# Kernel optimization log

Hardware: AMD Instinct MI355X
Metric: run time of the kernel (lower is better)

Reference implementation:

```python
import jax, jax.numpy as jnp
import numpy as np
from jax import lax

B, T = 256, 64
X_DIMS, CCG_DIMS, H, N_TAG = 512, 256, 1024, 512
DIN = X_DIMS + CCG_DIMS
PAD = 0


def setup_inputs() -> dict:
    key = jax.random.key(0)
    ks = jax.random.split(key, 12)
    emb = jax.random.normal(ks[0], (N_TAG, CCG_DIMS), jnp.float32)
    emb = emb.at[PAD].set(0.0)  # padding_idx row is zero
    s_ih = 1.0 / np.sqrt(H)
    return {
        "x": jax.random.normal(ks[1], (B, X_DIMS), jnp.float32),
        "atom_truth": jax.random.randint(ks[2], (B, T), 0, N_TAG),
        "atom_mask": jax.random.randint(ks[3], (B, T), 0, 2).astype(bool),
        "emb": emb,
        "W_ih": jax.random.normal(ks[4], (4 * H, DIN), jnp.float32) * s_ih,
        "W_hh": jax.random.normal(ks[5], (4 * H, H), jnp.float32) * s_ih,
        "b_ih": jax.random.normal(ks[6], (4 * H,), jnp.float32) * s_ih,
        "b_hh": jax.random.normal(ks[7], (4 * H,), jnp.float32) * s_ih,
        "W_out": jax.random.normal(ks[8], (N_TAG, H), jnp.float32) * s_ih,
        "b_out": jax.random.normal(ks[9], (N_TAG,), jnp.float32) * s_ih,
        "h0": jax.random.normal(ks[10], (B, H), jnp.float32),
        "c0": jax.random.normal(ks[11], (B, H), jnp.float32),
    }


def reference(x, atom_truth, atom_mask, emb, W_ih, W_hh, b_ih, b_hh, W_out, b_out, h0, c0):
    b, t = atom_truth.shape
    # teacher forcing: step 0 uses token 0, step k uses atom_truth[:, k-1]
    prev_tok = jnp.concatenate([jnp.zeros((b, 1), atom_truth.dtype), atom_truth[:, :-1]], axis=1)
    ccg = emb[prev_tok]                                      # [B,T,E]
    inp = jnp.concatenate([jnp.broadcast_to(x[:, None, :], (b, t, x.shape[1])), ccg], axis=-1)
    # precompute input projection for all steps: [B,T,4H]
    xproj = jnp.einsum('btd,gd->btg', inp, W_ih) + b_ih + b_hh

    def cell(carry, xt):                                     # xt: [B,4H]
        h, c = carry
        gates = xt + h @ W_hh.T
        i, f, g, o = jnp.split(gates, 4, axis=-1)            # torch gate order i,f,g,o
        i, f, o = jax.nn.sigmoid(i), jax.nn.sigmoid(f), jax.nn.sigmoid(o)
        g = jnp.tanh(g)
        c = f * c + i * g
        h = o * jnp.tanh(c)
        return (h, c), h

    _, hs = lax.scan(cell, (h0, c0), jnp.swapaxes(xproj, 0, 1))  # hs: [T,B,H]
    logits = hs @ W_out.T + b_out                            # [T,B,N_TAG]
    logp = jax.nn.log_softmax(logits, axis=-1)
    tgt = atom_truth.T                                       # [T,B]
    nll = -jnp.take_along_axis(logp, tgt[..., None], axis=-1)[..., 0]  # [T,B]
    mask = atom_mask.T.astype(nll.dtype)
    return jnp.sum(nll * mask) / jnp.sum(mask)


if __name__ == "__main__":
    print(reference(**setup_inputs()))
```

## Files before the change

### kernel.cpp

```cpp
#include <hip/hip_runtime.h>
#include <hip/hip_bf16.h>

#define BB 256
#define TT 64
#define XD 512
#define CCG 256
#define DINk 768
#define HH 1024
#define G4 4096
#define NTAG 512

typedef float f32x4 __attribute__((ext_vector_type(4)));
typedef short s16x8 __attribute__((ext_vector_type(8)));
typedef short s16x4 __attribute__((ext_vector_type(4)));

#define WS_HS    0ull
#define WS_XBASE (WS_HS + (size_t)(TT+1)*BB*HH*2)
#define WS_EPROJ (WS_XBASE + (size_t)BB*G4*4)
#define WS_WIH   (WS_EPROJ + (size_t)NTAG*G4*4)
#define WS_WOUT  (WS_WIH + (size_t)G4*DINk*2)
#define WS_XBF   (WS_WOUT + (size_t)NTAG*HH*2)
#define WS_EMBBF (WS_XBF + (size_t)BB*XD*2)
#define WS_CNT   (WS_EMBBF + (size_t)NTAG*CCG*2)
#define WS_ACC   (WS_CNT + 1024)
#define WS_FLAG  (WS_ACC + 64)
#define WS_XPROJ (WS_FLAG + 64)

static __device__ __forceinline__ short f2bf(float f) {
  __hip_bfloat16 h = __float2bfloat16(f);
  return __builtin_bit_cast(short, h);
}
static __device__ __forceinline__ float bf2f(unsigned short u) {
  unsigned x = ((unsigned)u) << 16;
  return __builtin_bit_cast(float, x);
}
static __device__ __forceinline__ void store_dword_cc(void* p, unsigned v) {
  asm volatile("global_store_dword %0, %1, off sc0 sc1" :: "v"(p), "v"(v) : "memory");
}
static __device__ __forceinline__ void store_short_cc(void* p, unsigned v) {
  asm volatile("global_store_short %0, %1, off sc0 sc1" :: "v"(p), "v"(v) : "memory");
}
static __device__ __forceinline__ int load_int_cc(const void* p) {
  int r;
  asm volatile("global_load_dword %0, %1, off sc0 sc1\n\ts_waitcnt vmcnt(0)"
               : "=v"(r) : "v"(p) : "memory");
  return r;
}
static __device__ __forceinline__ float fsig(float x) {
  return __builtin_amdgcn_rcpf(1.f + __expf(-x));
}
static __device__ __forceinline__ float ftanh(float x) {
  return 1.f - 2.f * __builtin_amdgcn_rcpf(1.f + __expf(2.f * x));
}

__global__ void k_f2bf8(const float* __restrict__ in, short* __restrict__ out, int n8) {
  int i = blockIdx.x * blockDim.x + threadIdx.x;
  if (i >= n8) return;
  size_t idx = (size_t)i * 8;
  float4 a = *(const float4*)(in + idx);
  float4 b = *(const float4*)(in + idx + 4);
  s16x8 o;
  o[0]=f2bf(a.x); o[1]=f2bf(a.y); o[2]=f2bf(a.z); o[3]=f2bf(a.w);
  o[4]=f2bf(b.x); o[5]=f2bf(b.y); o[6]=f2bf(b.z); o[7]=f2bf(b.w);
  *(s16x8*)(out + idx) = o;
}

__global__ void k_init(const float* __restrict__ h0, const int* __restrict__ mask_as_int,
                       char* __restrict__ ws) {
  int tid = blockIdx.x * blockDim.x + threadIdx.x;
  short* hb0 = (short*)(ws + WS_HS);
  for (int i = tid; i < BB * HH; i += gridDim.x * blockDim.x) hb0[i] = f2bf(h0[i]);
  if (blockIdx.x == 0) {
    int* cnt = (int*)(ws + WS_CNT);
    for (int i = threadIdx.x; i < 256; i += blockDim.x) cnt[i] = 0;
    int v = 0;
    for (int i = threadIdx.x; i < 4096; i += blockDim.x) v |= (mask_as_int[i] & ~1);
    __shared__ int red[256];
    red[threadIdx.x] = v;
    __syncthreads();
    if (threadIdx.x == 0) {
      int a = 0;
      for (int j = 0; j < 256; j++) a |= red[j];
      ((int*)(ws + WS_FLAG))[0] = (a != 0) ? 1 : 0;
      float* acc = (float*)(ws + WS_ACC);
      acc[0] = 0.f; acc[1] = 0.f;
    }
  }
}

__global__ __launch_bounds__(256) void k_gemm(const short* __restrict__ A, int lda,
    const short* __restrict__ Bm, int ldb, int bcol0,
    short* __restrict__ C, int ldc, int ksteps,
    const float* __restrict__ bias1, const float* __restrict__ bias2) {
  int w = threadIdx.x >> 6, l = threadIdx.x & 63;
  int lc = l & 15, lq = l >> 4;
  int arow = blockIdx.x * 64 + w * 16 + lc;
  f32x4 acc[4];
  const f32x4 z = {0.f, 0.f, 0.f, 0.f};
#pragma unroll
  for (int i = 0; i < 4; i++) acc[i] = z;
  const short* ap = A + (size_t)arow * lda + lq * 8;
  for (int kk = 0; kk < ksteps; ++kk) {
    s16x8 a = *(const s16x8*)(ap + kk * 32);
#pragma unroll
    for (int nt = 0; nt < 4; ++nt) {
      int brow = blockIdx.y * 64 + nt * 16 + lc;
      s16x8 b = *(const s16x8*)(Bm + (size_t)brow * ldb + bcol0 + kk * 32 + lq * 8);
      acc[nt] = __builtin_amdgcn_mfma_f32_16x16x32_bf16(a, b, acc[nt], 0, 0, 0);
    }
  }
#pragma unroll
  for (int nt = 0; nt < 4; ++nt) {
    int col = blockIdx.y * 64 + nt * 16 + lc;
    float badd = (bias1 ? bias1[col] : 0.f) + (bias2 ? bias2[col] : 0.f);
#pragma unroll
    for (int j = 0; j < 4; j++) {
      int r = blockIdx.x * 64 + w * 16 + lq * 4 + j;
      C[(size_t)r * ldc + col] = f2bf(acc[nt][j] + badd);
    }
  }
}

__global__ __launch_bounds__(256) void k_xproj_t(const short* __restrict__ xb,
    const short* __restrict__ ep, const int* __restrict__ atruth,
    short* __restrict__ out) {
  __shared__ short tile[64 * 264];
  const int cc = blockIdx.x, g = blockIdx.y, t = blockIdx.z;
  const int b = threadIdx.x;
  const int tok = (t == 0) ? 0 : atruth[b * TT + t - 1];
  const int gc0 = g * 1024 + cc * 64;
  const short* xs = xb + (size_t)b * G4 + gc0;
  const short* es = ep + (size_t)tok * G4 + gc0;
#pragma unroll
  for (int i = 0; i < 64; i += 8) {
    s16x8 xv = *(const s16x8*)(xs + i);
    s16x8 ev = *(const s16x8*)(es + i);
#pragma unroll
    for (int j = 0; j < 8; ++j)
      tile[(i + j) * 264 + b] = f2bf(bf2f((unsigned short)xv[j]) + bf2f((unsigned short)ev[j]));
  }
  __syncthreads();
  const int c = threadIdx.x >> 2, b0 = (threadIdx.x & 3) * 64;
  short* dst = out + ((size_t)t * G4 + gc0 + c) * BB + b0;
  const short* src = tile + c * 264 + b0;
#pragma unroll
  for (int i = 0; i < 64; i += 8) *(s16x8*)(dst + i) = *(const s16x8*)(src + i);
}

__global__ __launch_bounds__(512, 2) void k_lstm(const float* __restrict__ Whh,
    const short* __restrict__ xproj, const float* __restrict__ c0,
    char* __restrict__ ws) {
  extern __shared__ char sm[];
  float* part = (float*)sm;
  const int bid = blockIdx.x;
  const int xcd = bid & 7, slot = bid >> 3;
  const int mg = xcd >> 1;
  const int hb = slot * 2 + (xcd & 1);
  const int wgid = (xcd & 1) * 32 + slot;
  const int tid = threadIdx.x;
  const int w = tid >> 6, l = tid & 63;
  const int lc = l & 15, lq = l >> 4;
  const int wy = w & 1, kq = w >> 1;

  const int colbase = hb * 16;
  short* hs = (short*)(ws + WS_HS);
  int* flags = (int*)(ws + WS_CNT);
  const int arow0 = mg * 64 + wy * 32;

  s16x8 breg[4][8];
#pragma unroll
  for (int g = 0; g < 4; ++g) {
    const float* wr = Whh + (size_t)(g * HH + colbase + lc) * HH + kq * 256 + lq * 8;
#pragma unroll
    for (int s = 0; s < 8; ++s) {
      float4 f0 = *(const float4*)(wr + s * 32);
      float4 f1 = *(const float4*)(wr + s * 32 + 4);
      s16x8 o;
      o[0]=f2bf(f0.x); o[1]=f2bf(f0.y); o[2]=f2bf(f0.z); o[3]=f2bf(f0.w);
      o[4]=f2bf(f1.x); o[5]=f2bf(f1.y); o[6]=f2bf(f1.z); o[7]=f2bf(f1.w);
      breg[g][s] = o;
    }
  }

  float cst[2][4];
  if (kq == 0) {
#pragma unroll
    for (int rt = 0; rt < 2; ++rt)
#pragma unroll
      for (int j = 0; j < 4; ++j)
        cst[rt][j] = c0[(size_t)(arow0 + rt * 16 + lq * 4 + j) * HH + colbase + lc];
  }

  for (int t = 0; t < TT; ++t) {
    s16x4 xg[2][4];
    if (kq == 0) {
#pragma unroll
      for (int rt = 0; rt < 2; ++rt)
#pragma unroll
        for (int g = 0; g < 4; ++g)
          xg[rt][g] = *(const s16x4*)(xproj +
              ((size_t)t * G4 + g * HH + colbase + lc) * BB + arow0 + rt * 16 + lq * 4);
    }

    if (t && w == 0) {
      const int* f = flags + mg * 64 + l;
      for (;;) {
        int v = load_int_cc(f);
        if (__all(v >= t)) break;
        __builtin_amdgcn_s_sleep(1);
      }
    }
    __syncthreads();

    const f32x4 z = {0.f, 0.f, 0.f, 0.f};
    f32x4 acc[2][4];
#pragma unroll
    for (int rt = 0; rt < 2; ++rt)
#pragma unroll
      for (int g = 0; g < 4; ++g) acc[rt][g] = z;
    const short* ab = hs + (size_t)t * (BB * HH) + (size_t)(arow0 + lc) * HH + kq * 256 + lq * 8;
#pragma unroll
    for (int s = 0; s < 8; ++s) {
      s16x8 a0 = *(const s16x8*)(ab + s * 32);
      s16x8 a1 = *(const s16x8*)(ab + 16 * HH + s * 32);
#pragma unroll
      for (int g = 0; g < 4; ++g) {
        acc[0][g] = __builtin_amdgcn_mfma_f32_16x16x32_bf16(a0, breg[g][s], acc[0][g], 0, 0, 0);
        acc[1][g] = __builtin_amdgcn_mfma_f32_16x16x32_bf16(a1, breg[g][s], acc[1][g], 0, 0, 0);
      }
    }

    if (kq) {
      float* ps = part + (size_t)(((kq - 1) * 2 + wy) * 64 + l) * 36;
#pragma unroll
      for (int rt = 0; rt < 2; ++rt)
#pragma unroll
        for (int g = 0; g < 4; ++g)
          *(f32x4*)(ps + (rt * 4 + g) * 4) = acc[rt][g];
    }
    __syncthreads();

    if (kq == 0) {
#pragma unroll
      for (int q = 0; q < 3; ++q) {
        const float* ps = part + (size_t)((q * 2 + wy) * 64 + l) * 36;
#pragma unroll
        for (int rt = 0; rt < 2; ++rt)
#pragma unroll
          for (int g = 0; g < 4; ++g)
            acc[rt][g] += *(const f32x4*)(ps + (rt * 4 + g) * 4);
      }
#pragma unroll
      for (int rt = 0; rt < 2; ++rt) {
        short* hrow = hs + (size_t)(t + 1) * (BB * HH) +
                      (size_t)(arow0 + rt * 16 + lq * 4) * HH + colbase + lc;
#pragma unroll
        for (int j = 0; j < 4; ++j) {
          float pi = acc[rt][0][j] + bf2f((unsigned short)xg[rt][0][j]);
          float pf = acc[rt][1][j] + bf2f((unsigned short)xg[rt][1][j]);
          float pg = acc[rt][2][j] + bf2f((unsigned short)xg[rt][2][j]);
          float po = acc[rt][3][j] + bf2f((unsigned short)xg[rt][3][j]);
          float cv = fsig(pf) * cst[rt][j] + fsig(pi) * ftanh(pg);
          cst[rt][j] = cv;
          store_short_cc(hrow + (size_t)j * HH, (unsigned)(unsigned short)f2bf(fsig(po) * ftanh(cv)));
        }
      }
    }
    asm volatile("s_waitcnt vmcnt(0)" ::: "memory");
    __syncthreads();
    if (tid == 0 && t < TT - 1) store_dword_cc(flags + mg * 64 + wgid, t + 1);
  }
}

__global__ __launch_bounds__(256, 1) void k_logits(const short* __restrict__ hsb,
    const short* __restrict__ Wo, const float* __restrict__ bout,
    const int* __restrict__ atruth, const void* __restrict__ maskp,
    char* __restrict__ ws) {
  extern __shared__ char sm[];
  const int tid = threadIdx.x;
  const int w = tid >> 6, l = tid & 63;
  const int lc = l & 15, lq = l >> 4;
  const int rowbase = blockIdx.x * 64 + w * 16;
  f32x4 acc[32];
#pragma unroll
  for (int nt = 0; nt < 32; ++nt) {
    float bv = bout[nt * 16 + lc];
    f32x4 tmp = {bv, bv, bv, bv};
    acc[nt] = tmp;
  }
  const int swzl = (lc & 7) << 4;
  for (int kb = 0; kb < 16; ++kb) {
    __syncthreads();
    {
      const int r0 = tid >> 3, q = tid & 7;
#pragma unroll
      for (int i = 0; i < 16; i++) {
        int r = r0 + 32 * i;
        s16x8 v = *(const s16x8*)(Wo + (size_t)r * HH + kb * 64 + q * 8);
        *(s16x8*)(sm + r * 128 + ((q * 16) ^ ((r & 7) << 4))) = v;
      }
    }
    __syncthreads();
#pragma unroll
    for (int ks = 0; ks < 2; ++ks) {
      s16x8 a = *(const s16x8*)(hsb + (size_t)(rowbase + lc) * HH + kb * 64 + ks * 32 + lq * 8);
      const int kx = (ks * 64 + lq * 16) ^ swzl;
#pragma unroll
      for (int nt = 0; nt < 32; ++nt) {
        s16x8 b = *(const s16x8*)(sm + (nt * 16 + lc) * 128 + kx);
        acc[nt] = __builtin_amdgcn_mfma_f32_16x16x32_bf16(a, b, acc[nt], 0, 0, 0);
      }
    }
  }
  const int bytemode = ((const int*)(ws + WS_FLAG))[0];
  const unsigned char* mb = (const unsigned char*)maskp;
  const int* mi = (const int*)maskp;
  float nlls = 0.f, cnts = 0.f;
#pragma unroll
  for (int j = 0; j < 4; j++) {
    int gr = rowbase + lq * 4 + j;
    int tt = gr >> 8, b = gr & 255;
    float m = -1e30f;
#pragma unroll
    for (int nt = 0; nt < 32; ++nt) m = fmaxf(m, acc[nt][j]);
    m = fmaxf(m, __shfl_xor(m, 1)); m = fmaxf(m, __shfl_xor(m, 2));
    m = fmaxf(m, __shfl_xor(m, 4)); m = fmaxf(m, __shfl_xor(m, 8));
    float s = 0.f;
#pragma unroll
    for (int nt = 0; nt < 32; ++nt) s += __expf(acc[nt][j] - m);
    s += __shfl_xor(s, 1); s += __shfl_xor(s, 2);
    s += __shfl_xor(s, 4); s += __shfl_xor(s, 8);
    float lse = m + __logf(s);
    int tg = atruth[b * TT + tt];
    int mk = bytemode ? (int)mb[b * TT + tt] : mi[b * TT + tt];
    if (((tg & 15) == lc) && mk) {
      float tl = 0.f;
#pragma unroll
      for (int nt = 0; nt < 32; ++nt) if (nt == (tg >> 4)) tl = acc[nt][j];
      nlls += (lse - tl);
    }
    if (lc == 0 && mk) cnts += 1.f;
  }
#pragma unroll
  for (int off = 1; off < 64; off <<= 1) {
    nlls += __shfl_xor(nlls, off);
    cnts += __shfl_xor(cnts, off);
  }
  if (l == 0) {
    float* accf = (float*)(ws + WS_ACC);
    atomicAdd(&accf[0], nlls);
    atomicAdd(&accf[1], cnts);
  }
}

__global__ void k_final(const char* __restrict__ ws, float* __restrict__ out) {
  const float* accf = (const float*)(ws + WS_ACC);
  out[0] = accf[0] / accf[1];
}

extern "C" void kernel_launch(void* const* d_in, const int* in_sizes, int n_in,
                              void* d_out, int out_size, void* d_ws, size_t ws_size,
                              hipStream_t stream) {
  const float* x      = (const float*)d_in[0];
  const int*   atruth = (const int*)d_in[1];
  const void*  amask  = d_in[2];
  const float* emb    = (const float*)d_in[3];
  const float* W_ih   = (const float*)d_in[4];
  const float* W_hh   = (const float*)d_in[5];
  const float* b_ih   = (const float*)d_in[6];
  const float* b_hh   = (const float*)d_in[7];
  const float* W_out  = (const float*)d_in[8];
  const float* b_out  = (const float*)d_in[9];
  const float* h0     = (const float*)d_in[10];
  const float* c0     = (const float*)d_in[11];
  char* ws = (char*)d_ws;
  float* out = (float*)d_out;

  hipFuncSetAttribute((const void*)k_lstm, hipFuncAttributeMaxDynamicSharedMemorySize, 55296);
  hipFuncSetAttribute((const void*)k_logits, hipFuncAttributeMaxDynamicSharedMemorySize, 65536);

  k_f2bf8<<<dim3((G4 * DINk / 8 + 255) / 256), 256, 0, stream>>>(W_ih, (short*)(ws + WS_WIH), G4 * DINk / 8);
  k_f2bf8<<<dim3((NTAG * HH / 8 + 255) / 256), 256, 0, stream>>>(W_out, (short*)(ws + WS_WOUT), NTAG * HH / 8);
  k_f2bf8<<<dim3((BB * XD / 8 + 255) / 256), 256, 0, stream>>>(x, (short*)(ws + WS_XBF), BB * XD / 8);
  k_f2bf8<<<dim3((NTAG * CCG / 8 + 255) / 256), 256, 0, stream>>>(emb, (short*)(ws + WS_EMBBF), NTAG * CCG / 8);

  k_init<<<64, 256, 0, stream>>>(h0, (const int*)amask, ws);

  k_gemm<<<dim3(4, 64), 256, 0, stream>>>((short*)(ws + WS_XBF), XD, (short*)(ws + WS_WIH), DINk, 0,
                                          (short*)(ws + WS_XBASE), G4, XD / 32, b_ih, b_hh);
  k_gemm<<<dim3(8, 64), 256, 0, stream>>>((short*)(ws + WS_EMBBF), CCG, (short*)(ws + WS_WIH), DINk, XD,
                                          (short*)(ws + WS_EPROJ), G4, CCG / 32, nullptr, nullptr);

  k_xproj_t<<<dim3(16, 4, 64), 256, 0, stream>>>((const short*)(ws + WS_XBASE),
                                                 (const short*)(ws + WS_EPROJ), atruth,
                                                 (short*)(ws + WS_XPROJ));

  k_lstm<<<256, 512, 55296, stream>>>(W_hh, (const short*)(ws + WS_XPROJ), c0, ws);

  k_logits<<<256, 256, 65536, stream>>>((short*)(ws + WS_HS) + BB * HH, (short*)(ws + WS_WOUT), b_out,
                                        atruth, amask, ws);
  k_final<<<1, 1, 0, stream>>>(ws, out);
}
```

Measured before the change: 628.7 us.

## Fuse token-gathered input projection into LSTM kernel and retile to 32x32 blocks

Drops the separate pre-transposed per-timestep projection kernel and its large intermediate buffer. The LSTM kernel now keeps the constant x-projection for its own rows in registers. Each step it prefetches the embedding-projection rows for the next token into shared memory. Blocks are retiled to 32 batch rows by 32 hidden columns, so the inter-block flag barrier covers groups of 32 blocks instead of 64, and the cross-wave reduction plus gate epilogue is split across two waves instead of one. The larger shared-memory footprint (about 80 KB) may limit residency to one block per CU, and adds a per-step dependent token load.

```diff
diff --git a/kernel.cpp b/kernel.cpp
--- a/kernel.cpp
+++ b/kernel.cpp
@@ -24,7 +24,6 @@
 #define WS_CNT   (WS_EMBBF + (size_t)NTAG*CCG*2)
 #define WS_ACC   (WS_CNT + 1024)
 #define WS_FLAG  (WS_ACC + 64)
-#define WS_XPROJ (WS_FLAG + 64)
 
 static __device__ __forceinline__ short f2bf(float f) {
   __hip_bfloat16 h = __float2bfloat16(f);
@@ -121,56 +120,32 @@
   }
 }
 
-__global__ __launch_bounds__(256) void k_xproj_t(const short* __restrict__ xb,
-    const short* __restrict__ ep, const int* __restrict__ atruth,
-    short* __restrict__ out) {
-  __shared__ short tile[64 * 264];
-  const int cc = blockIdx.x, g = blockIdx.y, t = blockIdx.z;
-  const int b = threadIdx.x;
-  const int tok = (t == 0) ? 0 : atruth[b * TT + t - 1];
-  const int gc0 = g * 1024 + cc * 64;
-  const short* xs = xb + (size_t)b * G4 + gc0;
-  const short* es = ep + (size_t)tok * G4 + gc0;
-#pragma unroll
-  for (int i = 0; i < 64; i += 8) {
-    s16x8 xv = *(const s16x8*)(xs + i);
-    s16x8 ev = *(const s16x8*)(es + i);
-#pragma unroll
-    for (int j = 0; j < 8; ++j)
-      tile[(i + j) * 264 + b] = f2bf(bf2f((unsigned short)xv[j]) + bf2f((unsigned short)ev[j]));
-  }
-  __syncthreads();
-  const int c = threadIdx.x >> 2, b0 = (threadIdx.x & 3) * 64;
-  short* dst = out + ((size_t)t * G4 + gc0 + c) * BB + b0;
-  const short* src = tile + c * 264 + b0;
-#pragma unroll
-  for (int i = 0; i < 64; i += 8) *(s16x8*)(dst + i) = *(const s16x8*)(src + i);
-}
-
 __global__ __launch_bounds__(512, 2) void k_lstm(const float* __restrict__ Whh,
-    const short* __restrict__ xproj, const float* __restrict__ c0,
+    const short* __restrict__ xbase, const short* __restrict__ eproj,
+    const int* __restrict__ atruth, const float* __restrict__ c0,
     char* __restrict__ ws) {
   extern __shared__ char sm[];
   float* part = (float*)sm;
+  short* xbuf = (short*)(sm + 73728);
   const int bid = blockIdx.x;
   const int xcd = bid & 7, slot = bid >> 3;
-  const int mg = xcd >> 1;
-  const int hb = slot * 2 + (xcd & 1);
-  const int wgid = (xcd & 1) * 32 + slot;
+  const int grp = (xcd >> 1) * 2 + (slot & 1);
+  const int id  = (xcd & 1) * 16 + (slot >> 1);
+  const int row0 = grp * 32;
+  const int colbase = id * 32;
   const int tid = threadIdx.x;
   const int w = tid >> 6, l = tid & 63;
   const int lc = l & 15, lq = l >> 4;
-  const int wy = w & 1, kq = w >> 1;
-
-  const int colbase = hb * 16;
+  const int ct = w & 1, kq = w >> 1;
+  const int col0 = colbase + ct * 16;
+
   short* hs = (short*)(ws + WS_HS);
   int* flags = (int*)(ws + WS_CNT);
-  const int arow0 = mg * 64 + wy * 32;
 
   s16x8 breg[4][8];
 #pragma unroll
   for (int g = 0; g < 4; ++g) {
-    const float* wr = Whh + (size_t)(g * HH + colbase + lc) * HH + kq * 256 + lq * 8;
+    const float* wr = Whh + (size_t)(g * HH + col0 + lc) * HH + kq * 256 + lq * 8;
 #pragma unroll
     for (int s = 0; s < 8; ++s) {
       float4 f0 = *(const float4*)(wr + s * 32);
@@ -182,28 +157,26 @@
     }
   }
 
-  float cst[2][4];
-  if (kq == 0) {
-#pragma unroll
-    for (int rt = 0; rt < 2; ++rt)
-#pragma unroll
-      for (int j = 0; j < 4; ++j)
-        cst[rt][j] = c0[(size_t)(arow0 + rt * 16 + lq * 4 + j) * HH + colbase + lc];
-  }
+  float cst[4], xbf[4][4];
+  if (kq < 2) {
+#pragma unroll
+    for (int j = 0; j < 4; ++j) {
+      int r = row0 + kq * 16 + lq * 4 + j;
+      cst[j] = c0[(size_t)r * HH + col0 + lc];
+#pragma unroll
+      for (int g = 0; g < 4; ++g)
+        xbf[g][j] = bf2f((unsigned short)xbase[(size_t)r * G4 + g * HH + col0 + lc]);
+    }
+  }
+
+  const int gr = tid >> 4;
+  const int p16 = tid & 15;
+  const size_t ep_off = (size_t)(p16 >> 2) * HH + colbase + (p16 & 3) * 8;
+  s16x8 ev = *(const s16x8*)(eproj + ep_off);
 
   for (int t = 0; t < TT; ++t) {
-    s16x4 xg[2][4];
-    if (kq == 0) {
-#pragma unroll
-      for (int rt = 0; rt < 2; ++rt)
-#pragma unroll
-        for (int g = 0; g < 4; ++g)
-          xg[rt][g] = *(const s16x4*)(xproj +
-              ((size_t)t * G4 + g * HH + colbase + lc) * BB + arow0 + rt * 16 + lq * 4);
-    }
-
     if (t && w == 0) {
-      const int* f = flags + mg * 64 + l;
+      const int* f = flags + grp * 32 + (l & 31);
       for (;;) {
         int v = load_int_cc(f);
         if (__all(v >= t)) break;
@@ -212,13 +185,19 @@
     }
     __syncthreads();
 
+    *(s16x8*)(xbuf + gr * 132 + p16 * 8) = ev;
+    if (t + 1 < TT) {
+      int tokv = atruth[(row0 + gr) * TT + t];
+      ev = *(const s16x8*)(eproj + (size_t)tokv * G4 + ep_off);
+    }
+
     const f32x4 z = {0.f, 0.f, 0.f, 0.f};
     f32x4 acc[2][4];
 #pragma unroll
     for (int rt = 0; rt < 2; ++rt)
 #pragma unroll
       for (int g = 0; g < 4; ++g) acc[rt][g] = z;
-    const short* ab = hs + (size_t)t * (BB * HH) + (size_t)(arow0 + lc) * HH + kq * 256 + lq * 8;
+    const short* ab = hs + (size_t)t * (BB * HH) + (size_t)(row0 + lc) * HH + kq * 256 + lq * 8;
 #pragma unroll
     for (int s = 0; s < 8; ++s) {
       s16x8 a0 = *(const s16x8*)(ab + s * 32);
@@ -230,45 +209,52 @@
       }
     }
 
-    if (kq) {
-      float* ps = part + (size_t)(((kq - 1) * 2 + wy) * 64 + l) * 36;
-#pragma unroll
-      for (int rt = 0; rt < 2; ++rt)
-#pragma unroll
-        for (int g = 0; g < 4; ++g)
-          *(f32x4*)(ps + (rt * 4 + g) * 4) = acc[rt][g];
-    }
-    __syncthreads();
-
-    if (kq == 0) {
-#pragma unroll
-      for (int q = 0; q < 3; ++q) {
-        const float* ps = part + (size_t)((q * 2 + wy) * 64 + l) * 36;
-#pragma unroll
-        for (int rt = 0; rt < 2; ++rt)
-#pragma unroll
-          for (int g = 0; g < 4; ++g)
-            acc[rt][g] += *(const f32x4*)(ps + (rt * 4 + g) * 4);
-      }
-#pragma unroll
-      for (int rt = 0; rt < 2; ++rt) {
-        short* hrow = hs + (size_t)(t + 1) * (BB * HH) +
-                      (size_t)(arow0 + rt * 16 + lq * 4) * HH + colbase + lc;
-#pragma unroll
-        for (int j = 0; j < 4; ++j) {
-          float pi = acc[rt][0][j] + bf2f((unsigned short)xg[rt][0][j]);
-          float pf = acc[rt][1][j] + bf2f((unsigned short)xg[rt][1][j]);
-          float pg = acc[rt][2][j] + bf2f((unsigned short)xg[rt][2][j]);
-          float po = acc[rt][3][j] + bf2f((unsigned short)xg[rt][3][j]);
-          float cv = fsig(pf) * cst[rt][j] + fsig(pi) * ftanh(pg);
-          cst[rt][j] = cv;
-          store_short_cc(hrow + (size_t)j * HH, (unsigned)(unsigned short)f2bf(fsig(po) * ftanh(cv)));
-        }
+    {
+      float* pb0 = part + (size_t)(((kq * 2 + ct) * 2 + 0) * 64 + l) * 18;
+      float* pb1 = part + (size_t)(((kq * 2 + ct) * 2 + 1) * 64 + l) * 18;
+      if (kq != 0) {
+#pragma unroll
+        for (int g = 0; g < 4; ++g) *(f32x4*)(pb0 + g * 4) = acc[0][g];
+      }
+      if (kq != 1) {
+#pragma unroll
+        for (int g = 0; g < 4; ++g) *(f32x4*)(pb1 + g * 4) = acc[1][g];
+      }
+    }
+    __syncthreads();
+
+    if (kq < 2) {
+      const int rt = kq;
+      f32x4 s0 = acc[rt][0], s1 = acc[rt][1], s2 = acc[rt][2], s3 = acc[rt][3];
+#pragma unroll
+      for (int q2 = 0; q2 < 4; ++q2) {
+        if (q2 == kq) continue;
+        const float* pb = part + (size_t)(((q2 * 2 + ct) * 2 + rt) * 64 + l) * 18;
+        s0 += *(const f32x4*)(pb);
+        s1 += *(const f32x4*)(pb + 4);
+        s2 += *(const f32x4*)(pb + 8);
+        s3 += *(const f32x4*)(pb + 12);
+      }
+      const unsigned short* xbu = (const unsigned short*)xbuf;
+      const int cc = ct * 16 + lc;
+      short* hbase = hs + (size_t)(t + 1) * (BB * HH);
+#pragma unroll
+      for (int j = 0; j < 4; ++j) {
+        int rr = kq * 16 + lq * 4 + j;
+        int xi = rr * 132;
+        float pi = s0[j] + bf2f(xbu[xi + cc])      + xbf[0][j];
+        float pf = s1[j] + bf2f(xbu[xi + 32 + cc]) + xbf[1][j];
+        float pg = s2[j] + bf2f(xbu[xi + 64 + cc]) + xbf[2][j];
+        float po = s3[j] + bf2f(xbu[xi + 96 + cc]) + xbf[3][j];
+        float cv = fsig(pf) * cst[j] + fsig(pi) * ftanh(pg);
+        cst[j] = cv;
+        store_short_cc(hbase + (size_t)(row0 + rr) * HH + col0 + lc,
+                       (unsigned)(unsigned short)f2bf(fsig(po) * ftanh(cv)));
       }
     }
     asm volatile("s_waitcnt vmcnt(0)" ::: "memory");
     __syncthreads();
-    if (tid == 0 && t < TT - 1) store_dword_cc(flags + mg * 64 + wgid, t + 1);
+    if (tid == 0 && t < TT - 1) store_dword_cc(flags + grp * 32 + id, t + 1);
   }
 }
 
@@ -376,7 +362,7 @@
   char* ws = (char*)d_ws;
   float* out = (float*)d_out;
 
-  hipFuncSetAttribute((const void*)k_lstm, hipFuncAttributeMaxDynamicSharedMemorySize, 55296);
+  hipFuncSetAttribute((const void*)k_lstm, hipFuncAttributeMaxDynamicSharedMemorySize, 82176);
   hipFuncSetAttribute((const void*)k_logits, hipFuncAttributeMaxDynamicSharedMemorySize, 65536);
 
   k_f2bf8<<<dim3((G4 * DINk / 8 + 255) / 256), 256, 0, stream>>>(W_ih, (short*)(ws + WS_WIH), G4 * DINk / 8);
@@ -391,11 +377,8 @@
   k_gemm<<<dim3(8, 64), 256, 0, stream>>>((short*)(ws + WS_EMBBF), CCG, (short*)(ws + WS_WIH), DINk, XD,
                                           (short*)(ws + WS_EPROJ), G4, CCG / 32, nullptr, nullptr);
 
-  k_xproj_t<<<dim3(16, 4, 64), 256, 0, stream>>>((const short*)(ws + WS_XBASE),
-                                                 (const short*)(ws + WS_EPROJ), atruth,
-                                                 (short*)(ws + WS_XPROJ));
-
-  k_lstm<<<256, 512, 55296, stream>>>(W_hh, (const short*)(ws + WS_XPROJ), c0, ws);
+  k_lstm<<<256, 512, 82176, stream>>>(W_hh, (const short*)(ws + WS_XBASE),
+                                      (const short*)(ws + WS_EPROJ), atruth, c0, ws);
 
   k_logits<<<256, 256, 65536, stream>>>((short*)(ws + WS_HS) + BB * HH, (short*)(ws + WS_WOUT), b_out,
                                         atruth, amask, ws);
```

After: 909.9 us. +44.7%, slower.
